# Kernel tuning notes

Measured on AMD Instinct MI355X. Metric: run time of the kernel, lower is better.

Reference implementation:

```python
import jax, jax.numpy as jnp
import numpy as np

H, C, L = 4, 64, 3          # heads, out_channels, conv layers
N, E, B = 20000, 320000, 32 # nodes, edges, graphs
HD = 64                     # hidden_dim


def setup_inputs() -> dict:
    key = jax.random.key(0)
    ks = jax.random.split(key, 24)
    x = jax.random.normal(ks[0], (N, 3), jnp.float32)
    src = jax.random.randint(ks[1], (E,), 0, N)
    dst = jax.random.randint(ks[2], (E,), 0, N)
    dst = jnp.where(dst == src, (dst + 1) % N, dst)  # no pre-existing self loops
    edge_index = jnp.stack([src, dst])
    edge_attr = jax.random.normal(ks[3], (E, 4), jnp.float32)
    u = jax.random.normal(ks[4], (B, 10), jnp.float32)
    batch = jnp.sort(jax.random.randint(ks[5], (N,), 0, B))
    p = lambda k, s: jax.random.normal(k, s, jnp.float32) * 0.1
    return {
        'x': x, 'edge_index': edge_index, 'edge_attr': edge_attr, 'u': u, 'batch': batch,
        'node_W': p(ks[6], (3, HD)), 'node_b': p(ks[7], (HD,)),
        'eemb_W': p(ks[8], (4, HD)), 'eemb_b': p(ks[9], (HD,)),
        'lin_W': p(ks[10], (L, HD, H * C)),
        'att_src': p(ks[11], (L, H, C)), 'att_dst': p(ks[12], (L, H, C)),
        'lin_eW': p(ks[13], (L, HD, H * C)), 'att_e': p(ks[14], (L, H, C)),
        'conv_b': p(ks[15], (L, C)),
        'gW': p(ks[16], (10, HD)), 'gb': p(ks[17], (HD,)),
        'f1W': p(ks[18], (2 * HD, HD)), 'f1b': p(ks[19], (HD,)),
        'f2W': p(ks[20], (HD, 2)), 'f2b': p(ks[21], (2,)),
    }


def _gat_layer(x, src, dst, ea, W, a_src, a_dst, We, a_e, b):
    # PyG GATConv(hidden, hidden, edge_dim=hidden, heads=4, concat=False), eval mode
    n = x.shape[0]
    # add self loops; self-loop edge_attr = mean of incoming edge_attr (fill_value='mean')
    deg = jax.ops.segment_sum(jnp.ones_like(dst, dtype=x.dtype), dst, num_segments=n)
    ea_self = jax.ops.segment_sum(ea, dst, num_segments=n) / jnp.maximum(deg, 1.0)[:, None]
    loop = jnp.arange(n)
    src2 = jnp.concatenate([src, loop])
    dst2 = jnp.concatenate([dst, loop])
    ea2 = jnp.concatenate([ea, ea_self], axis=0)
    xp = (x @ W).reshape(n, H, C)                       # [N,H,C]
    a_s = jnp.einsum('nhc,hc->nh', xp, a_src)           # [N,H]
    a_d = jnp.einsum('nhc,hc->nh', xp, a_dst)
    ee = (ea2 @ We).reshape(-1, H, C)                   # [E2,H,C]
    a_ed = jnp.einsum('ehc,hc->eh', ee, a_e)
    alpha = jax.nn.leaky_relu(a_s[src2] + a_d[dst2] + a_ed, 0.2)  # [E2,H]
    # segment softmax over destination nodes (stable)
    m = jax.ops.segment_max(alpha, dst2, num_segments=n)
    ex = jnp.exp(alpha - m[dst2])
    den = jax.ops.segment_sum(ex, dst2, num_segments=n)
    att = ex / den[dst2]
    out = jax.ops.segment_sum(xp[src2] * att[..., None], dst2, num_segments=n)  # [N,H,C]
    return out.mean(axis=1) + b  # concat=False -> mean over heads


def reference(x, edge_index, edge_attr, u, batch, node_W, node_b, eemb_W, eemb_b,
              lin_W, att_src, att_dst, lin_eW, att_e, conv_b, gW, gb, f1W, f1b, f2W, f2b):
    src, dst = edge_index[0], edge_index[1]
    h = jax.nn.relu(x @ node_W + node_b)
    ea = jax.nn.relu(edge_attr @ eemb_W + eemb_b)
    for i in range(L):
        h = jax.nn.relu(_gat_layer(h, src, dst, ea, lin_W[i], att_src[i], att_dst[i],
                                   lin_eW[i], att_e[i], conv_b[i]))
    # global mean pool over graphs
    cnt = jax.ops.segment_sum(jnp.ones((h.shape[0],), h.dtype), batch, num_segments=B)
    pooled = jax.ops.segment_sum(h, batch, num_segments=B) / jnp.maximum(cnt, 1.0)[:, None]
    ug = jax.nn.relu(u @ gW + gb)
    z = jnp.concatenate([pooled, ug], axis=1)
    z = jax.nn.relu(z @ f1W + f1b)
    return z @ f2W + f2b
```

## Files before the change

kernel.cpp:

```cpp
#include <hip/hip_runtime.h>
#include <hip/hip_bf16.h>

#define HD 64

typedef unsigned short u16;

__device__ __forceinline__ float lrelu(float x) { return x > 0.f ? x : 0.2f * x; }
__device__ __forceinline__ int clampi(int v, int maxv) {
    return v < 0 ? 0 : (v >= maxv ? maxv - 1 : v);
}
__device__ __forceinline__ float bf2f(u16 u) {
    return __uint_as_float(((unsigned int)u) << 16);
}
__device__ __forceinline__ u16 f2bf(float f) {
    unsigned int u = __float_as_uint(f);
    unsigned int lsb = (u >> 16) & 1u;
    u += 0x7fffu + lsb;
    return (u16)(u >> 16);
}

__global__ void k_init(int* deg, int* cursor, int* gcnt, float* pooled, int N, int B) {
    int i = blockIdx.x * blockDim.x + threadIdx.x;
    if (i < N) { deg[i] = 0; cursor[i] = 0; }
    if (i < B) gcnt[i] = 0;
    if (i < B * HD) pooled[i] = 0.f;
}

__global__ void k_node_emb(const float* __restrict__ x, const float* __restrict__ W,
                           const float* __restrict__ b, float* __restrict__ h, int N) {
    int i = blockIdx.x * blockDim.x + threadIdx.x;
    if (i >= N * HD) return;
    int n = i >> 6, c = i & 63;
    float acc = b[c];
    acc = fmaf(x[n * 3 + 0], W[0 * HD + c], acc);
    acc = fmaf(x[n * 3 + 1], W[1 * HD + c], acc);
    acc = fmaf(x[n * 3 + 2], W[2 * HD + c], acc);
    h[i] = fmaxf(acc, 0.f);
}

__global__ void k_deg(const int* __restrict__ dst, int* __restrict__ deg, int E, int N) {
    int e = blockIdx.x * blockDim.x + threadIdx.x;
    if (e < E) atomicAdd(&deg[clampi(dst[e], N)], 1);
}

__global__ void k_scan1(const int* __restrict__ deg, int* __restrict__ tmp,
                        int* __restrict__ bsum, int N) {
    __shared__ int s[256];
    int tid = threadIdx.x;
    int i = blockIdx.x * 256 + tid;
    int v = (i < N) ? deg[i] : 0;
    s[tid] = v;
    __syncthreads();
    for (int off = 1; off < 256; off <<= 1) {
        int t = (tid >= off) ? s[tid - off] : 0;
        __syncthreads();
        s[tid] += t;
        __syncthreads();
    }
    if (i < N) tmp[i] = s[tid];
    if (tid == 255) bsum[blockIdx.x] = s[255];
}
__global__ void k_scan2(const int* __restrict__ bsum, int* __restrict__ boff, int nb) {
    __shared__ int s[1024];
    int tid = threadIdx.x;
    int v = (tid < nb) ? bsum[tid] : 0;
    s[tid] = v;
    __syncthreads();
    for (int off = 1; off < 1024; off <<= 1) {
        int t = (tid >= off) ? s[tid - off] : 0;
        __syncthreads();
        s[tid] += t;
        __syncthreads();
    }
    if (tid < nb) boff[tid] = s[tid] - v;
}
__global__ void k_scan3(const int* __restrict__ tmp, const int* __restrict__ boff,
                        int* __restrict__ row_ptr, int N) {
    int i = blockIdx.x * blockDim.x + threadIdx.x;
    if (i == 0) row_ptr[0] = 0;
    if (i < N) row_ptr[i + 1] = tmp[i] + boff[i >> 8];
}

__global__ void k_csr(const int* __restrict__ src, const int* __restrict__ dst,
                      const int* __restrict__ row_ptr, int* __restrict__ cursor,
                      int* __restrict__ csr_src, int* __restrict__ csr_dst,
                      int* __restrict__ csr_eid, int E, int N) {
    int e = blockIdx.x * blockDim.x + threadIdx.x;
    if (e >= E) return;
    int d = clampi(dst[e], N);
    int pos = row_ptr[d] + atomicAdd(&cursor[d], 1);
    if (pos < E) {
        csr_src[pos] = clampi(src[e], N);
        csr_dst[pos] = d;
        csr_eid[pos] = e;
    }
}

#define MAXB 2048
__global__ void k_gse(const int* __restrict__ batch, int* __restrict__ gcnt, int N, int B) {
    __shared__ int s_cnt[MAXB];
    int t = threadIdx.x;
    int Bc = B < MAXB ? B : MAXB;
    for (int i = t; i < Bc; i += blockDim.x) s_cnt[i] = 0;
    __syncthreads();
    int n = blockIdx.x * blockDim.x + t;
    if (n < N) {
        int b = clampi(batch[n], B);
        if (b < MAXB) atomicAdd(&s_cnt[b], 1);
        else atomicAdd(&gcnt[b], 1);
    }
    __syncthreads();
    for (int i = t; i < Bc; i += blockDim.x)
        if (s_cnt[i] != 0) atomicAdd(&gcnt[i], s_cnt[i]);
}

__global__ __launch_bounds__(256) void k_eaself(
    const float* __restrict__ edge_attr, const float* __restrict__ eW,
    const float* __restrict__ eB, const int* __restrict__ row_ptr,
    const int* __restrict__ csr_eid, float* __restrict__ ea_self, int N) {
    int wave = threadIdx.x >> 6, lane = threadIdx.x & 63;
    int n = blockIdx.x * 4 + wave;
    if (n >= N) return;
    float w0 = eW[0 * HD + lane], w1 = eW[1 * HD + lane];
    float w2 = eW[2 * HD + lane], w3 = eW[3 * HD + lane];
    float bb = eB[lane];
    int r0 = row_ptr[n], r1 = row_ptr[n + 1];
    float acc = 0.f;
    for (int j = r0; j < r1; j++) {
        int e = csr_eid[j];
        float a0 = edge_attr[e * 4 + 0], a1 = edge_attr[e * 4 + 1];
        float a2 = edge_attr[e * 4 + 2], a3 = edge_attr[e * 4 + 3];
        float v = fmaf(a0, w0, fmaf(a1, w1, fmaf(a2, w2, fmaf(a3, w3, bb))));
        acc += fmaxf(v, 0.f);
    }
    ea_self[n * HD + lane] = acc / fmaxf((float)(r1 - r0), 1.f);
}

__global__ __launch_bounds__(256) void k_xp(
    const float* __restrict__ h, const float* __restrict__ W,
    const float* __restrict__ asrc, const float* __restrict__ adst,
    u16* __restrict__ xp, float* __restrict__ a_s, float* __restrict__ a_d, int N) {
    __shared__ float hs[8 * HD];
    int n0 = blockIdx.x * 8;
    int t = threadIdx.x;
    for (int i = t; i < 8 * HD; i += 256) {
        int nn = n0 + (i >> 6);
        hs[i] = (nn < N) ? h[(size_t)nn * HD + (i & 63)] : 0.f;
    }
    __syncthreads();
    int c = t;
    float acc[8];
    #pragma unroll
    for (int k = 0; k < 8; k++) acc[k] = 0.f;
    for (int d = 0; d < HD; d++) {
        float wv = W[d * 256 + c];
        #pragma unroll
        for (int k = 0; k < 8; k++) acc[k] = fmaf(hs[k * HD + d], wv, acc[k]);
    }
    float as_ = asrc[c], ad_ = adst[c];
    int hh = c >> 6, cc = c & 63;
    #pragma unroll
    for (int k = 0; k < 8; k++) {
        int nn = n0 + k;
        float ps = acc[k] * as_;
        float pd = acc[k] * ad_;
        #pragma unroll
        for (int o = 32; o > 0; o >>= 1) {
            ps += __shfl_xor(ps, o);
            pd += __shfl_xor(pd, o);
        }
        if (nn < N) {
            xp[(size_t)nn * 256 + c] = f2bf(acc[k]);
            if (cc == 0) { a_s[nn * 4 + hh] = ps; a_d[nn * 4 + hh] = pd; }
        }
    }
}

__global__ __launch_bounds__(256) void k_w(
    const float* __restrict__ edge_attr, const float* __restrict__ eW,
    const float* __restrict__ eB, const float* __restrict__ We,
    const float* __restrict__ ae, const float* __restrict__ ea_self,
    const int* __restrict__ csr_src, const int* __restrict__ csr_dst,
    const int* __restrict__ csr_eid, const float* __restrict__ a_s,
    const float* __restrict__ a_d, float* __restrict__ wcsr, int E, int N) {
    __shared__ float s_wred[256];
    __shared__ float s_ew[256];
    __shared__ float s_eb[64];
    int t = threadIdx.x;
    {
        int h = t >> 6, d = t & 63;
        float acc = 0.f;
        for (int c = 0; c < 64; c++)
            acc = fmaf(We[d * 256 + h * 64 + c], ae[h * 64 + c], acc);
        s_wred[t] = acc;
        s_ew[t] = eW[t];
        if (t < 64) s_eb[t] = eB[t];
    }
    __syncthreads();
    int j = blockIdx.x * blockDim.x + t;
    float h0 = 0.f, h1 = 0.f, h2 = 0.f, h3 = 0.f;
    int s, d;
    if (j < E) {
        int e = csr_eid[j];
        float4 a = *(const float4*)(edge_attr + (size_t)e * 4);
        for (int k = 0; k < HD; k++) {
            float v = fmaf(a.x, s_ew[k], fmaf(a.y, s_ew[64 + k],
                      fmaf(a.z, s_ew[128 + k], fmaf(a.w, s_ew[192 + k], s_eb[k]))));
            v = fmaxf(v, 0.f);
            h0 = fmaf(v, s_wred[k], h0);
            h1 = fmaf(v, s_wred[64 + k], h1);
            h2 = fmaf(v, s_wred[128 + k], h2);
            h3 = fmaf(v, s_wred[192 + k], h3);
        }
        s = csr_src[j];
        d = csr_dst[j];
    } else if (j < E + N) {
        int n = j - E;
        for (int k = 0; k < HD; k++) {
            float v = ea_self[n * HD + k];
            h0 = fmaf(v, s_wred[k], h0);
            h1 = fmaf(v, s_wred[64 + k], h1);
            h2 = fmaf(v, s_wred[128 + k], h2);
            h3 = fmaf(v, s_wred[192 + k], h3);
        }
        s = n;
        d = n;
    } else {
        return;
    }
    float4 as4 = *(const float4*)(a_s + s * 4);
    float4 ad4 = *(const float4*)(a_d + d * 4);
    float w0 = __expf(lrelu(as4.x + ad4.x + h0));
    float w1 = __expf(lrelu(as4.y + ad4.y + h1));
    float w2 = __expf(lrelu(as4.z + ad4.z + h2));
    float w3 = __expf(lrelu(as4.w + ad4.w + h3));
    *(float4*)(wcsr + (size_t)j * 4) = make_float4(w0, w1, w2, w3);
}

__global__ __launch_bounds__(256) void k_gat(
    const u16* __restrict__ xp, const float* __restrict__ wcsr,
    const int* __restrict__ row_ptr, const int* __restrict__ csr_src,
    const float* __restrict__ convb, float* __restrict__ h_out, int N, int E) {
    int wave = threadIdx.x >> 6, lane = threadIdx.x & 63;
    int n = blockIdx.x * 4 + wave;
    if (n >= N) return;
    int g = lane >> 4, p = lane & 15;
    int r0 = row_ptr[n], r1 = row_ptr[n + 1];
    float a00 = 0.f, a01 = 0.f, a02 = 0.f, a03 = 0.f;
    float a10 = 0.f, a11 = 0.f, a12 = 0.f, a13 = 0.f;
    float a20 = 0.f, a21 = 0.f, a22 = 0.f, a23 = 0.f;
    float a30 = 0.f, a31 = 0.f, a32 = 0.f, a33 = 0.f;
    float d0 = 0.f, d1 = 0.f, d2 = 0.f, d3 = 0.f;
    if (g == 0) {
        float4 w = *(const float4*)(wcsr + (size_t)(E + n) * 4);
        const u16* row = xp + (size_t)n * 256 + p * 4;
        ushort4 v0 = *(const ushort4*)(row);
        ushort4 v1 = *(const ushort4*)(row + 64);
        ushort4 v2 = *(const ushort4*)(row + 128);
        ushort4 v3 = *(const ushort4*)(row + 192);
        d0 += w.x; d1 += w.y; d2 += w.z; d3 += w.w;
        a00 = fmaf(w.x, bf2f(v0.x), a00); a01 = fmaf(w.x, bf2f(v0.y), a01);
        a02 = fmaf(w.x, bf2f(v0.z), a02); a03 = fmaf(w.x, bf2f(v0.w), a03);
        a10 = fmaf(w.y, bf2f(v1.x), a10); a11 = fmaf(w.y, bf2f(v1.y), a11);
        a12 = fmaf(w.y, bf2f(v1.z), a12); a13 = fmaf(w.y, bf2f(v1.w), a13);
        a20 = fmaf(w.z, bf2f(v2.x), a20); a21 = fmaf(w.z, bf2f(v2.y), a21);
        a22 = fmaf(w.z, bf2f(v2.z), a22); a23 = fmaf(w.z, bf2f(v2.w), a23);
        a30 = fmaf(w.w, bf2f(v3.x), a30); a31 = fmaf(w.w, bf2f(v3.y), a31);
        a32 = fmaf(w.w, bf2f(v3.z), a32); a33 = fmaf(w.w, bf2f(v3.w), a33);
    }
    for (int j = r0 + g; j < r1; j += 4) {
        float4 w = *(const float4*)(wcsr + (size_t)j * 4);
        const u16* row = xp + (size_t)csr_src[j] * 256 + p * 4;
        ushort4 v0 = *(const ushort4*)(row);
        ushort4 v1 = *(const ushort4*)(row + 64);
        ushort4 v2 = *(const ushort4*)(row + 128);
        ushort4 v3 = *(const ushort4*)(row + 192);
        d0 += w.x; d1 += w.y; d2 += w.z; d3 += w.w;
        a00 = fmaf(w.x, bf2f(v0.x), a00); a01 = fmaf(w.x, bf2f(v0.y), a01);
        a02 = fmaf(w.x, bf2f(v0.z), a02); a03 = fmaf(w.x, bf2f(v0.w), a03);
        a10 = fmaf(w.y, bf2f(v1.x), a10); a11 = fmaf(w.y, bf2f(v1.y), a11);
        a12 = fmaf(w.y, bf2f(v1.z), a12); a13 = fmaf(w.y, bf2f(v1.w), a13);
        a20 = fmaf(w.z, bf2f(v2.x), a20); a21 = fmaf(w.z, bf2f(v2.y), a21);
        a22 = fmaf(w.z, bf2f(v2.z), a22); a23 = fmaf(w.z, bf2f(v2.w), a23);
        a30 = fmaf(w.w, bf2f(v3.x), a30); a31 = fmaf(w.w, bf2f(v3.y), a31);
        a32 = fmaf(w.w, bf2f(v3.z), a32); a33 = fmaf(w.w, bf2f(v3.w), a33);
    }
    d0 += __shfl_xor(d0, 16); d0 += __shfl_xor(d0, 32);
    d1 += __shfl_xor(d1, 16); d1 += __shfl_xor(d1, 32);
    d2 += __shfl_xor(d2, 16); d2 += __shfl_xor(d2, 32);
    d3 += __shfl_xor(d3, 16); d3 += __shfl_xor(d3, 32);
    float i0 = 1.f / d0, i1 = 1.f / d1, i2 = 1.f / d2, i3 = 1.f / d3;
    float m0 = a00 * i0 + a10 * i1 + a20 * i2 + a30 * i3;
    float m1 = a01 * i0 + a11 * i1 + a21 * i2 + a31 * i3;
    float m2 = a02 * i0 + a12 * i1 + a22 * i2 + a32 * i3;
    float m3 = a03 * i0 + a13 * i1 + a23 * i2 + a33 * i3;
    m0 += __shfl_xor(m0, 16); m0 += __shfl_xor(m0, 32);
    m1 += __shfl_xor(m1, 16); m1 += __shfl_xor(m1, 32);
    m2 += __shfl_xor(m2, 16); m2 += __shfl_xor(m2, 32);
    m3 += __shfl_xor(m3, 16); m3 += __shfl_xor(m3, 32);
    if (lane < 16) {
        int c = p * 4;
        h_out[(size_t)n * HD + c + 0] = fmaxf(0.25f * m0 + convb[c + 0], 0.f);
        h_out[(size_t)n * HD + c + 1] = fmaxf(0.25f * m1 + convb[c + 1], 0.f);
        h_out[(size_t)n * HD + c + 2] = fmaxf(0.25f * m2 + convb[c + 2], 0.f);
        h_out[(size_t)n * HD + c + 3] = fmaxf(0.25f * m3 + convb[c + 3], 0.f);
    }
}

__global__ void k_pool(const float* __restrict__ h, const int* __restrict__ batch,
                       float* __restrict__ pooled, int N, int B) {
    int i = blockIdx.x * blockDim.x + threadIdx.x;
    if (i >= N * HD) return;
    int n = i >> 6, c = i & 63;
    int b = clampi(batch[n], B);
    atomicAdd(&pooled[b * HD + c], h[i]);
}

__global__ void k_mlp(const float* __restrict__ u, const float* __restrict__ gW,
                      const float* __restrict__ gb, const float* __restrict__ pooled,
                      const int* __restrict__ gcnt, const float* __restrict__ f1W,
                      const float* __restrict__ f1b, const float* __restrict__ f2W,
                      const float* __restrict__ f2b, float* __restrict__ out, int B) {
    __shared__ float z[2 * HD];
    __shared__ float z1s[HD];
    int b = blockIdx.x, t = threadIdx.x;
    float acc = gb[t];
    for (int k = 0; k < 10; k++) acc = fmaf(u[b * 10 + k], gW[k * HD + t], acc);
    z[HD + t] = fmaxf(acc, 0.f);
    float invc = 1.f / fmaxf((float)gcnt[b], 1.f);
    z[t] = pooled[b * HD + t] * invc;
    __syncthreads();
    float a1 = f1b[t];
    for (int k = 0; k < 2 * HD; k++) a1 = fmaf(z[k], f1W[k * HD + t], a1);
    z1s[t] = fmaxf(a1, 0.f);
    __syncthreads();
    if (t < 2) {
        float o = f2b[t];
        for (int k = 0; k < HD; k++) o = fmaf(z1s[k], f2W[k * 2 + t], o);
        out[b * 2 + t] = o;
    }
}

extern "C" void kernel_launch(void* const* d_in, const int* in_sizes, int n_in,
                              void* d_out, int out_size, void* d_ws, size_t ws_size,
                              hipStream_t stream) {
    const float* x         = (const float*)d_in[0];
    const int*   ei        = (const int*)d_in[1];
    const float* edge_attr = (const float*)d_in[2];
    const float* u         = (const float*)d_in[3];
    const int*   batch     = (const int*)d_in[4];
    const float* node_W    = (const float*)d_in[5];
    const float* node_b    = (const float*)d_in[6];
    const float* eemb_W    = (const float*)d_in[7];
    const float* eemb_b    = (const float*)d_in[8];
    const float* lin_W     = (const float*)d_in[9];
    const float* att_src   = (const float*)d_in[10];
    const float* att_dst   = (const float*)d_in[11];
    const float* lin_eW    = (const float*)d_in[12];
    const float* att_e     = (const float*)d_in[13];
    const float* conv_b    = (const float*)d_in[14];
    const float* gW        = (const float*)d_in[15];
    const float* gb        = (const float*)d_in[16];
    const float* f1W       = (const float*)d_in[17];
    const float* f1b       = (const float*)d_in[18];
    const float* f2W       = (const float*)d_in[19];
    const float* f2b       = (const float*)d_in[20];

    const int N = in_sizes[0] / 3;
    const int E = in_sizes[2] / 4;
    const int B = in_sizes[3] / 10;
    const int* src = ei;
    const int* dst = ei + E;
    const int NB = (N + 255) / 256;

    float* wsf = (float*)d_ws;
    float* h       = wsf;              wsf += (size_t)N * HD;
    float* a_s     = wsf;              wsf += (size_t)N * 4;
    float* a_d     = wsf;              wsf += (size_t)N * 4;
    float* ea_self = wsf;              wsf += (size_t)N * HD;
    float* wcsr    = wsf;              wsf += (size_t)(E + N) * 4;
    float* pooled  = wsf;              wsf += (size_t)B * HD;
    u16* xp = (u16*)wsf;               wsf += (size_t)N * 128;
    int* wsi = (int*)wsf;
    int* deg     = wsi;                wsi += N;
    int* row_ptr = wsi;                wsi += N + 1;
    int* cursor  = wsi;                wsi += N;
    int* tmp     = wsi;                wsi += N;
    int* bsum    = wsi;                wsi += NB + 1;
    int* boff    = wsi;                wsi += NB + 1;
    int* csr_src = wsi;                wsi += E;
    int* csr_dst = wsi;                wsi += E;
    int* csr_eid = wsi;                wsi += E;
    int* gcnt    = wsi;                wsi += B;

    k_init<<<NB, 256, 0, stream>>>(deg, cursor, gcnt, pooled, N, B);
    k_node_emb<<<(N * HD + 255) / 256, 256, 0, stream>>>(x, node_W, node_b, h, N);
    k_deg<<<(E + 255) / 256, 256, 0, stream>>>(dst, deg, E, N);
    k_scan1<<<NB, 256, 0, stream>>>(deg, tmp, bsum, N);
    k_scan2<<<1, 1024, 0, stream>>>(bsum, boff, NB);
    k_scan3<<<NB, 256, 0, stream>>>(tmp, boff, row_ptr, N);
    k_csr<<<(E + 255) / 256, 256, 0, stream>>>(src, dst, row_ptr, cursor,
                                               csr_src, csr_dst, csr_eid, E, N);
    k_gse<<<NB, 256, 0, stream>>>(batch, gcnt, N, B);
    k_eaself<<<(N + 3) / 4, 256, 0, stream>>>(edge_attr, eemb_W, eemb_b, row_ptr, csr_eid,
                                              ea_self, N);
    for (int i = 0; i < 3; i++) {
        k_xp<<<(N + 7) / 8, 256, 0, stream>>>(h, lin_W + (size_t)i * HD * 256,
                                              att_src + (size_t)i * 256,
                                              att_dst + (size_t)i * 256,
                                              xp, a_s, a_d, N);
        k_w<<<(E + N + 255) / 256, 256, 0, stream>>>(
            edge_attr, eemb_W, eemb_b, lin_eW + (size_t)i * HD * 256,
            att_e + (size_t)i * 256, ea_self, csr_src, csr_dst, csr_eid,
            a_s, a_d, wcsr, E, N);
        k_gat<<<(N + 3) / 4, 256, 0, stream>>>(xp, wcsr, row_ptr, csr_src,
                                               conv_b + (size_t)i * HD, h, N, E);
    }
    k_pool<<<(N * HD + 255) / 256, 256, 0, stream>>>(h, batch, pooled, N, B);
    k_mlp<<<B, 64, 0, stream>>>(u, gW, gb, pooled, gcnt, f1W, f1b, f2W, f2b,
                                (float*)d_out, B);
}
```

Before: 457.7 us.

## Precompute per-edge attention edge terms for all layers once

```diff
diff --git a/kernel.cpp b/kernel.cpp
--- a/kernel.cpp
+++ b/kernel.cpp
@@ -114,26 +114,64 @@
         if (s_cnt[i] != 0) atomicAdd(&gcnt[i], s_cnt[i]);
 }
 
-__global__ __launch_bounds__(256) void k_eaself(
+__global__ __launch_bounds__(256) void k_ee(
     const float* __restrict__ edge_attr, const float* __restrict__ eW,
-    const float* __restrict__ eB, const int* __restrict__ row_ptr,
-    const int* __restrict__ csr_eid, float* __restrict__ ea_self, int N) {
-    int wave = threadIdx.x >> 6, lane = threadIdx.x & 63;
-    int n = blockIdx.x * 4 + wave;
+    const float* __restrict__ eB, const float* __restrict__ lin_eW,
+    const float* __restrict__ att_e, const int* __restrict__ csr_eid,
+    float* __restrict__ aed, int E) {
+    __shared__ float s_ew[256];
+    __shared__ float s_eb[64];
+    __shared__ float s_wred[768];
+    int t = threadIdx.x;
+    s_ew[t] = eW[t];
+    if (t < 64) s_eb[t] = eB[t];
+    for (int idx = t; idx < 768; idx += 256) {
+        int l = idx >> 8, hd = idx & 255, hh = hd >> 6, d = hd & 63;
+        const float* We = lin_eW + (size_t)l * HD * 256;
+        const float* ae = att_e + (size_t)l * 256;
+        float acc = 0.f;
+        for (int c = 0; c < 64; c++)
+            acc = fmaf(We[d * 256 + hh * 64 + c], ae[hh * 64 + c], acc);
+        s_wred[idx] = acc;
+    }
+    __syncthreads();
+    int j = blockIdx.x * blockDim.x + t;
+    if (j >= E) return;
+    int e = csr_eid[j];
+    float4 a = *(const float4*)(edge_attr + (size_t)e * 4);
+    float acc[12];
+    #pragma unroll
+    for (int m = 0; m < 12; m++) acc[m] = 0.f;
+    for (int k = 0; k < HD; k++) {
+        float v = fmaf(a.x, s_ew[k], fmaf(a.y, s_ew[64 + k],
+                  fmaf(a.z, s_ew[128 + k], fmaf(a.w, s_ew[192 + k], s_eb[k]))));
+        v = fmaxf(v, 0.f);
+        #pragma unroll
+        for (int m = 0; m < 12; m++)
+            acc[m] = fmaf(v, s_wred[(m >> 2) * 256 + (m & 3) * 64 + k], acc[m]);
+    }
+    float* o = aed + (size_t)j * 12;
+    #pragma unroll
+    for (int m = 0; m < 12; m++) o[m] = acc[m];
+}
+
+__global__ void k_selfed(const int* __restrict__ row_ptr, float* __restrict__ aed,
+                         int E, int N) {
+    int n = blockIdx.x * blockDim.x + threadIdx.x;
     if (n >= N) return;
-    float w0 = eW[0 * HD + lane], w1 = eW[1 * HD + lane];
-    float w2 = eW[2 * HD + lane], w3 = eW[3 * HD + lane];
-    float bb = eB[lane];
     int r0 = row_ptr[n], r1 = row_ptr[n + 1];
-    float acc = 0.f;
+    float acc[12];
+    #pragma unroll
+    for (int m = 0; m < 12; m++) acc[m] = 0.f;
     for (int j = r0; j < r1; j++) {
-        int e = csr_eid[j];
-        float a0 = edge_attr[e * 4 + 0], a1 = edge_attr[e * 4 + 1];
-        float a2 = edge_attr[e * 4 + 2], a3 = edge_attr[e * 4 + 3];
-        float v = fmaf(a0, w0, fmaf(a1, w1, fmaf(a2, w2, fmaf(a3, w3, bb))));
-        acc += fmaxf(v, 0.f);
-    }
-    ea_self[n * HD + lane] = acc / fmaxf((float)(r1 - r0), 1.f);
+        const float* p = aed + (size_t)j * 12;
+        #pragma unroll
+        for (int m = 0; m < 12; m++) acc[m] += p[m];
+    }
+    float inv = 1.f / fmaxf((float)(r1 - r0), 1.f);
+    float* o = aed + (size_t)(E + n) * 12;
+    #pragma unroll
+    for (int m = 0; m < 12; m++) o[m] = acc[m] * inv;
 }
 
 __global__ __launch_bounds__(256) void k_xp(
@@ -176,64 +214,22 @@
     }
 }
 
-__global__ __launch_bounds__(256) void k_w(
-    const float* __restrict__ edge_attr, const float* __restrict__ eW,
-    const float* __restrict__ eB, const float* __restrict__ We,
-    const float* __restrict__ ae, const float* __restrict__ ea_self,
-    const int* __restrict__ csr_src, const int* __restrict__ csr_dst,
-    const int* __restrict__ csr_eid, const float* __restrict__ a_s,
-    const float* __restrict__ a_d, float* __restrict__ wcsr, int E, int N) {
-    __shared__ float s_wred[256];
-    __shared__ float s_ew[256];
-    __shared__ float s_eb[64];
-    int t = threadIdx.x;
-    {
-        int h = t >> 6, d = t & 63;
-        float acc = 0.f;
-        for (int c = 0; c < 64; c++)
-            acc = fmaf(We[d * 256 + h * 64 + c], ae[h * 64 + c], acc);
-        s_wred[t] = acc;
-        s_ew[t] = eW[t];
-        if (t < 64) s_eb[t] = eB[t];
-    }
-    __syncthreads();
-    int j = blockIdx.x * blockDim.x + t;
-    float h0 = 0.f, h1 = 0.f, h2 = 0.f, h3 = 0.f;
+__global__ void k_w(const int* __restrict__ csr_src, const int* __restrict__ csr_dst,
+                    const float* __restrict__ aed, const float* __restrict__ a_s,
+                    const float* __restrict__ a_d, float* __restrict__ wcsr,
+                    int layer, int E, int N) {
+    int j = blockIdx.x * blockDim.x + threadIdx.x;
+    if (j >= E + N) return;
     int s, d;
-    if (j < E) {
-        int e = csr_eid[j];
-        float4 a = *(const float4*)(edge_attr + (size_t)e * 4);
-        for (int k = 0; k < HD; k++) {
-            float v = fmaf(a.x, s_ew[k], fmaf(a.y, s_ew[64 + k],
-                      fmaf(a.z, s_ew[128 + k], fmaf(a.w, s_ew[192 + k], s_eb[k]))));
-            v = fmaxf(v, 0.f);
-            h0 = fmaf(v, s_wred[k], h0);
-            h1 = fmaf(v, s_wred[64 + k], h1);
-            h2 = fmaf(v, s_wred[128 + k], h2);
-            h3 = fmaf(v, s_wred[192 + k], h3);
-        }
-        s = csr_src[j];
-        d = csr_dst[j];
-    } else if (j < E + N) {
-        int n = j - E;
-        for (int k = 0; k < HD; k++) {
-            float v = ea_self[n * HD + k];
-            h0 = fmaf(v, s_wred[k], h0);
-            h1 = fmaf(v, s_wred[64 + k], h1);
-            h2 = fmaf(v, s_wred[128 + k], h2);
-            h3 = fmaf(v, s_wred[192 + k], h3);
-        }
-        s = n;
-        d = n;
-    } else {
-        return;
-    }
+    if (j < E) { s = csr_src[j]; d = csr_dst[j]; }
+    else       { s = j - E; d = s; }
+    const float* p = aed + (size_t)j * 12 + layer * 4;
     float4 as4 = *(const float4*)(a_s + s * 4);
     float4 ad4 = *(const float4*)(a_d + d * 4);
-    float w0 = __expf(lrelu(as4.x + ad4.x + h0));
-    float w1 = __expf(lrelu(as4.y + ad4.y + h1));
-    float w2 = __expf(lrelu(as4.z + ad4.z + h2));
-    float w3 = __expf(lrelu(as4.w + ad4.w + h3));
+    float w0 = __expf(lrelu(as4.x + ad4.x + p[0]));
+    float w1 = __expf(lrelu(as4.y + ad4.y + p[1]));
+    float w2 = __expf(lrelu(as4.z + ad4.z + p[2]));
+    float w3 = __expf(lrelu(as4.w + ad4.w + p[3]));
     *(float4*)(wcsr + (size_t)j * 4) = make_float4(w0, w1, w2, w3);
 }
 
@@ -377,7 +373,7 @@
     float* h       = wsf;              wsf += (size_t)N * HD;
     float* a_s     = wsf;              wsf += (size_t)N * 4;
     float* a_d     = wsf;              wsf += (size_t)N * 4;
-    float* ea_self = wsf;              wsf += (size_t)N * HD;
+    float* aed     = wsf;              wsf += (size_t)(E + N) * 12;
     float* wcsr    = wsf;              wsf += (size_t)(E + N) * 4;
     float* pooled  = wsf;              wsf += (size_t)B * HD;
     u16* xp = (u16*)wsf;               wsf += (size_t)N * 128;
@@ -402,17 +398,16 @@
     k_csr<<<(E + 255) / 256, 256, 0, stream>>>(src, dst, row_ptr, cursor,
                                                csr_src, csr_dst, csr_eid, E, N);
     k_gse<<<NB, 256, 0, stream>>>(batch, gcnt, N, B);
-    k_eaself<<<(N + 3) / 4, 256, 0, stream>>>(edge_attr, eemb_W, eemb_b, row_ptr, csr_eid,
-                                              ea_self, N);
+    k_ee<<<(E + 255) / 256, 256, 0, stream>>>(edge_attr, eemb_W, eemb_b, lin_eW, att_e,
+                                              csr_eid, aed, E);
+    k_selfed<<<NB, 256, 0, stream>>>(row_ptr, aed, E, N);
     for (int i = 0; i < 3; i++) {
         k_xp<<<(N + 7) / 8, 256, 0, stream>>>(h, lin_W + (size_t)i * HD * 256,
                                               att_src + (size_t)i * 256,
                                               att_dst + (size_t)i * 256,
                                               xp, a_s, a_d, N);
-        k_w<<<(E + N + 255) / 256, 256, 0, stream>>>(
-            edge_attr, eemb_W, eemb_b, lin_eW + (size_t)i * HD * 256,
-            att_e + (size_t)i * 256, ea_self, csr_src, csr_dst, csr_eid,
-            a_s, a_d, wcsr, E, N);
+        k_w<<<(E + N + 255) / 256, 256, 0, stream>>>(csr_src, csr_dst, aed, a_s, a_d,
+                                                     wcsr, i, E, N);
         k_gat<<<(N + 3) / 4, 256, 0, stream>>>(xp, wcsr, row_ptr, csr_src,
                                                conv_b + (size_t)i * HD, h, N, E);
     }
```

Result: faster. 422.4 us (-7.7%).
